# Performance work log

Measured on AMD Instinct MI355X. Metric: run time of the kernel, lower is better.

The kernel has to match this reference:

```python
import jax, jax.numpy as jnp
import numpy as np

BN_EPS = 1e-5


def setup_inputs() -> dict:
    key = jax.random.key(0)
    ks = jax.random.split(key, 9)
    N, C, T, V, S, INTER, OUT = 64, 64, 300, 25, 3, 16, 64
    return {
        "x": jax.random.normal(ks[0], (N, C, T, V), dtype=jnp.float32),
        "A": jax.random.uniform(ks[1], (S, V, V), dtype=jnp.float32),
        "PA": jax.random.normal(ks[2], (S, V, V), dtype=jnp.float32) * 1e-3,
        "Wa": jax.random.normal(ks[3], (S, INTER, C), dtype=jnp.float32) * 0.1,
        "ba": jax.random.normal(ks[4], (S, INTER), dtype=jnp.float32) * 0.1,
        "Wb": jax.random.normal(ks[5], (S, INTER, C), dtype=jnp.float32) * 0.1,
        "bb": jax.random.normal(ks[6], (S, INTER), dtype=jnp.float32) * 0.1,
        "Wd": jax.random.normal(ks[7], (S, OUT, C), dtype=jnp.float32) * 0.1,
        "bd": jax.random.normal(ks[8], (S, OUT), dtype=jnp.float32) * 0.1,
        "gamma": jnp.ones((OUT,), dtype=jnp.float32),
        "beta": jnp.zeros((OUT,), dtype=jnp.float32),
    }


def reference(x, A, PA, Wa, ba, Wb, bb, Wd, bd, gamma, beta):
    N, C, T, V = x.shape
    S, INTER = Wa.shape[0], Wa.shape[1]
    K = INTER * T  # contraction length for attention

    # 1x1 convs for all subsets at once: [N,S,inter,T,V]
    fa = jnp.einsum('nctv,sic->nsitv', x, Wa) + ba[None, :, :, None, None]
    fb = jnp.einsum('nctv,sic->nsitv', x, Wb) + bb[None, :, :, None, None]

    # A1: permute(0,3,1,2).view(N,V,inter*T)  -> [N,S,V,K]
    A1 = fa.transpose(0, 1, 4, 2, 3).reshape(N, S, V, K)
    # A2: view(N,inter*T,V)                   -> [N,S,K,V]
    A2 = fb.reshape(N, S, K, V)

    # attention: softmax over dim=-2, plus learned adjacency
    att = jnp.einsum('nsvk,nskw->nsvw', A1, A2) / jnp.asarray(K, x.dtype)
    att = jax.nn.softmax(att, axis=-2) + (A + PA)[None]  # [N,S,V,V]

    # message passing: x.view(N,C*T,V) @ att, then 1x1 conv_d, summed over subsets
    xm = jnp.einsum('nkv,nsvw->nskw', x.reshape(N, C * T, V), att)
    xm = xm.reshape(N, S, C, T, V)
    y = jnp.einsum('nsctv,soc->notv', xm, Wd) + bd.sum(0)[None, :, None, None]

    # BatchNorm2d (training-mode batch stats, per-channel over N,T,V)
    mean = y.mean(axis=(0, 2, 3), keepdims=True)
    var = y.var(axis=(0, 2, 3), keepdims=True)
    y = gamma[None, :, None, None] * (y - mean) * jax.lax.rsqrt(var + BN_EPS) \
        + beta[None, :, None, None]

    # residual (in_channels == out_channels -> identity down) + relu
    return jax.nn.relu(y + x)
```

## Files before the change

### kernel.cpp

```cpp
#include <hip/hip_runtime.h>
#include <math.h>

constexpr int Nn = 64, Cc = 64, Tt = 300, Vv = 25, Ss = 3, Ii = 16, Oo = 64;
constexpr int TVc  = Tt * Vv;
constexpr int CTVc = Cc * TVc;
constexpr float KINV = 1.0f / 4800.0f;

constexpr int WS_ATT  = 0;
constexpr int WS_SUM  = 120000;
constexpr int WS_SQ   = 120512;
constexpr int WS_MEAN = 121024;
constexpr int WS_RSTD = 121088;
constexpr int WS_ZERO_FLOATS = 121024;
constexpr int WS_XB_F   = 121152;
constexpr int WS_WAB_F  = WS_XB_F + 15360000;
constexpr int WS_WDB_F  = WS_WAB_F + 3072;
constexpr int WS_ATTB_F = WS_WDB_F + 6144;
constexpr int WS_END_F  = WS_ATTB_F + 98304;
constexpr size_t WS_NEED = (size_t)WS_END_F * 4;

typedef __attribute__((ext_vector_type(8))) short bf16x8;
typedef __attribute__((ext_vector_type(4))) short short4v;
typedef __attribute__((ext_vector_type(4))) float f32x4;
typedef __attribute__((ext_vector_type(16))) float f32x16;
typedef __attribute__((ext_vector_type(4))) int int4v;

__device__ __forceinline__ short f2bf(float f) {
    unsigned u = __builtin_bit_cast(unsigned, f);
    u += 0x7FFFu + ((u >> 16) & 1u);
    return (short)(u >> 16);
}
__device__ __forceinline__ float bf2f(short s) {
    unsigned u = ((unsigned)(unsigned short)s) << 16;
    return __builtin_bit_cast(float, u);
}
__device__ __forceinline__ void store4(float* p, f32x4 v) {
    __builtin_memcpy(p, &v, 16);
}

__global__ __launch_bounds__(256) void k0_xpose(
    const float* __restrict__ x, short* __restrict__ xb)
{
    const int n   = blockIdx.y;
    const int tid = threadIdx.x;
    const int tv  = blockIdx.x * 32 + (tid & 31);
    const int g   = (tid >> 5) & 7;
    if (tv >= TVc) return;
    const float* xp = x + (size_t)n * CTVc + (size_t)(g * 8) * TVc + tv;
    bf16x8 o;
    #pragma unroll
    for (int j = 0; j < 8; ++j) o[j] = f2bf(xp[(size_t)j * TVc]);
    *(bf16x8*)(xb + ((size_t)n * TVc + tv) * 64 + g * 8) = o;
}

__global__ __launch_bounds__(256) void kpack(
    const float* __restrict__ Wa, const float* __restrict__ Wb,
    const float* __restrict__ Wd, short* __restrict__ wab, short* __restrict__ wdb)
{
    const int i = blockIdx.x * 256 + threadIdx.x;
    if (i < 6144) {
        const int s = i >> 11, rb = i & 2047, r = rb >> 6, c = rb & 63;
        const float v = (r < 16) ? Wa[(s * 16 + r) * 64 + c]
                                 : Wb[(s * 16 + (r - 16)) * 64 + c];
        wab[i] = f2bf(v);
    }
    if (i < 12288) wdb[i] = f2bf(Wd[i]);
}

template<bool XB>
__device__ __forceinline__ void load_xfrag(
    const float* __restrict__ xn, const short* __restrict__ xbn,
    int tv, bool ok, int quad, bf16x8& b0, bf16x8& b1)
{
    if constexpr (XB) {
        const short* bp = xbn + (ok ? tv : 0) * 64 + quad * 8;
        b0 = *(const bf16x8*)bp;
        b1 = *(const bf16x8*)(bp + 32);
    } else {
        const float* bp = xn + (quad * 8) * TVc + tv;
        #pragma unroll
        for (int j = 0; j < 8; ++j) {
            b0[j] = f2bf(ok ? bp[j * TVc] : 0.0f);
            b1[j] = f2bf(ok ? bp[(j + 32) * TVc] : 0.0f);
        }
    }
}

template<bool XB>
__global__ __launch_bounds__(256) void ka_gram_mfma(
    const float* __restrict__ x, const short* __restrict__ xb,
    const short* __restrict__ wab,
    const float* __restrict__ Wa, const float* __restrict__ ba,
    const float* __restrict__ Wb, const float* __restrict__ bb,
    float* __restrict__ att)
{
    __shared__ short uT[112 * 104];
    __shared__ float part[4 * 1024];
    __shared__ float bab[96];

    const int tid = threadIdx.x;
    const int t0  = blockIdx.x * 4;
    const int n   = blockIdx.y;
    const float* xn  = x + n * CTVc + t0 * 25;
    const short* xbn = XB ? (xb + ((size_t)n * TVc + t0 * 25) * 64) : nullptr;

    if (tid < 96) {
        const int s = tid >> 5, r = tid & 31;
        bab[tid] = (r < 16) ? ba[s * 16 + r] : bb[s * 16 + r - 16];
    }

    const int lane = tid & 63;
    const int wave = tid >> 6;
    const int l16  = lane & 15;
    const int quad = lane >> 4;

    bf16x8 afr[3][2][2];
    #pragma unroll
    for (int s = 0; s < 3; ++s)
        #pragma unroll
        for (int half = 0; half < 2; ++half)
            #pragma unroll
            for (int k = 0; k < 2; ++k) {
                if constexpr (XB) {
                    afr[s][half][k] = *(const bf16x8*)(
                        wab + (s * 32 + half * 16 + l16) * 64 + k * 32 + quad * 8);
                } else {
                    const float* W = half ? Wb : Wa;
                    const float* wp = W + (s * 16 + l16) * 64 + k * 32 + quad * 8;
                    const float4 w0 = *(const float4*)wp;
                    const float4 w1 = *(const float4*)(wp + 4);
                    bf16x8 a;
                    a[0] = f2bf(w0.x); a[1] = f2bf(w0.y); a[2] = f2bf(w0.z); a[3] = f2bf(w0.w);
                    a[4] = f2bf(w1.x); a[5] = f2bf(w1.y); a[6] = f2bf(w1.z); a[7] = f2bf(w1.w);
                    afr[s][half][k] = a;
                }
            }
    __syncthreads();

    for (int nt = wave; nt < 7; nt += 4) {
        const int tv = nt * 16 + l16;
        const bool ok = tv < 100;
        bf16x8 b0, b1;
        load_xfrag<XB>(xn, xbn, tv, ok, quad, b0, b1);
        #pragma unroll
        for (int s = 0; s < 3; ++s)
            #pragma unroll
            for (int half = 0; half < 2; ++half) {
                f32x4 acc = {0.0f, 0.0f, 0.0f, 0.0f};
                acc = __builtin_amdgcn_mfma_f32_16x16x32_bf16(afr[s][half][0], b0, acc, 0, 0, 0);
                acc = __builtin_amdgcn_mfma_f32_16x16x32_bf16(afr[s][half][1], b1, acc, 0, 0, 0);
                const float4 bv = *(const float4*)(bab + s * 32 + half * 16 + quad * 4);
                short4v pk;
                pk[0] = f2bf(acc[0] + bv.x); pk[1] = f2bf(acc[1] + bv.y);
                pk[2] = f2bf(acc[2] + bv.z); pk[3] = f2bf(acc[3] + bv.w);
                *(short4v*)(uT + tv * 104 + s * 32 + half * 16 + quad * 4) = pk;
            }
    }
    __syncthreads();

    const int t   = wave;
    const int w32 = lane & 31;
    const int khi = lane >> 5;
    f32x16 g[3];
    #pragma unroll
    for (int s = 0; s < 3; ++s)
        #pragma unroll
        for (int r = 0; r < 16; ++r) g[s][r] = 0.0f;

    #pragma unroll
    for (int s = 0; s < 3; ++s) {
        const short* base = uT + (t * 25 + w32) * 104 + s * 32 + khi * 8;
        const bf16x8 aA = *(const bf16x8*)(base);
        const bf16x8 bB = *(const bf16x8*)(base + 16);
        g[s] = __builtin_amdgcn_mfma_f32_32x32x16_bf16(aA, bB, g[s], 0, 0, 0);
    }

    for (int s = 0; s < 3; ++s) {
        __syncthreads();
        #pragma unroll
        for (int r = 0; r < 16; ++r) {
            const int row = (r & 3) + 8 * (r >> 2) + 4 * khi;
            part[wave * 1024 + row * 32 + w32] = g[s][r];
        }
        __syncthreads();
        float* attns = att + (n * 3 + s) * 625;
        for (int p = tid; p < 625; p += 256) {
            const int v = p / 25, w = p - v * 25;
            const int q = v * 32 + w;
            atomicAdd(attns + p, part[q] + part[1024 + q] + part[2048 + q] + part[3072 + q]);
        }
    }
}

template<bool ATTB>
__global__ __launch_bounds__(64) void kb_softmax(
    float* __restrict__ att, const float* __restrict__ A, const float* __restrict__ PA,
    short* __restrict__ attb)
{
    const int b = blockIdx.x;
    const int s = b % 3;
    const int w = threadIdx.x;
    if (w >= 32) return;
    float col[25] = {};
    if (w < 25) {
        float* base = att + b * 625;
        float m = -1e30f;
        #pragma unroll
        for (int v = 0; v < 25; ++v) {
            col[v] = base[v * 25 + w] * KINV;
            m = fmaxf(m, col[v]);
        }
        float sum = 0.0f;
        #pragma unroll
        for (int v = 0; v < 25; ++v) { col[v] = expf(col[v] - m); sum += col[v]; }
        const float inv = 1.0f / sum;
        #pragma unroll
        for (int v = 0; v < 25; ++v) {
            col[v] = fmaf(col[v], inv, A[(s * 25 + v) * 25 + w] + PA[(s * 25 + v) * 25 + w]);
            base[v * 25 + w] = col[v];
        }
    }
    if constexpr (ATTB) {
        short* dst = attb + b * 1024 + w * 32;
        #pragma unroll
        for (int v = 0; v < 25; ++v) dst[v] = (w < 25) ? f2bf(col[v]) : (short)0;
        #pragma unroll
        for (int v = 25; v < 32; ++v) dst[v] = 0;
    }
}

constexpr int K3_TILES = 3;

__global__ __launch_bounds__(512, 6) void k3_y_mfma(
    const short* __restrict__ xb, const short* __restrict__ wdb,
    const short* __restrict__ attb, float* __restrict__ y, float* __restrict__ bns)
{
    __shared__ __align__(16) short U[192 * 128];
    __shared__ float bnA[8][32], bnB[8][32];

    const int tid = threadIdx.x;
    const int n   = blockIdx.y;
    const int tb0 = blockIdx.x * K3_TILES;

    const int lane = tid & 63;
    const int wave = tid >> 6;
    const int l16  = lane & 15;
    const int quad = lane >> 4;

    for (int i = tid; i < 3072; i += 512)
        ((int4v*)U)[i] = (int4v){0, 0, 0, 0};

    bf16x8 a0[3], a1[3];
    #pragma unroll
    for (int s = 0; s < 3; ++s) {
        const short* ab = attb + (size_t)(n * 3 + s) * 1024 + l16 * 32 + quad * 8;
        a0[s] = *(const bf16x8*)ab;
        a1[s] = *(const bf16x8*)(ab + 512);
    }

    const int tv  = (wave < 7) ? wave * 16 + l16 : 0;
    const bool ok = (wave < 7) && (tv < 100);
    const int tl  = tv / 25;
    const int vp  = tv - tl * 25;
    const int col = tl * 32 + vp;
    const int grp = col >> 3, ing = col & 7;

    const short* xtile = xb + ((size_t)n * TVc + tb0 * 100) * 64;
    const int xoff = (ok ? tv : 0) * 64 + quad * 8;

    bf16x8 bc0 = *(const bf16x8*)(xtile + xoff);
    bf16x8 bc1 = *(const bf16x8*)(xtile + xoff + 32);
    bf16x8 nx0, nx1;

    const int t  = wave >> 1;
    const int ob = (wave & 1) * 32;
    float s1[2] = {0.0f, 0.0f}, s2[2] = {0.0f, 0.0f};

    __syncthreads();

    #pragma unroll
    for (int it = 0; it < K3_TILES; ++it) {
        if (it + 1 < K3_TILES) {
            const short* bp = xtile + (it + 1) * 6400 + xoff;
            nx0 = *(const bf16x8*)bp;
            nx1 = *(const bf16x8*)(bp + 32);
        }

        if (wave < 7) {
            #pragma unroll
            for (int s = 0; s < 3; ++s)
                #pragma unroll
                for (int m = 0; m < 4; ++m) {
                    const short* wp = wdb + (s * 64 + m * 16 + l16) * 64 + quad * 8;
                    const bf16x8 f0 = *(const bf16x8*)wp;
                    const bf16x8 f1 = *(const bf16x8*)(wp + 32);
                    f32x4 acc = {0.0f, 0.0f, 0.0f, 0.0f};
                    acc = __builtin_amdgcn_mfma_f32_16x16x32_bf16(f0, bc0, acc, 0, 0, 0);
                    acc = __builtin_amdgcn_mfma_f32_16x16x32_bf16(f1, bc1, acc, 0, 0, 0);
                    if (ok) {
                        #pragma unroll
                        for (int r = 0; r < 4; ++r) {
                            const int row = s * 64 + m * 16 + quad * 4 + r;
                            U[row * 128 + (((grp ^ (row & 15)) << 3) | ing)] = f2bf(acc[r]);
                        }
                    }
                }
        }
        __syncthreads();

        f32x4 D[2][2];
        #pragma unroll
        for (int mt = 0; mt < 2; ++mt)
            #pragma unroll
            for (int nb = 0; nb < 2; ++nb) D[mt][nb] = (f32x4){0.0f, 0.0f, 0.0f, 0.0f};
        #pragma unroll
        for (int s = 0; s < 3; ++s) {
            #pragma unroll
            for (int nb = 0; nb < 2; ++nb) {
                const int row = s * 64 + ob + nb * 16 + l16;
                const bf16x8 bv = *(const bf16x8*)(
                    U + row * 128 + (((t * 4 + quad) ^ (row & 15)) << 3));
                D[0][nb] = __builtin_amdgcn_mfma_f32_16x16x32_bf16(a0[s], bv, D[0][nb], 0, 0, 0);
                D[1][nb] = __builtin_amdgcn_mfma_f32_16x16x32_bf16(a1[s], bv, D[1][nb], 0, 0, 0);
            }
        }

        const int t0 = (tb0 + it) * 4;
        #pragma unroll
        for (int nb = 0; nb < 2; ++nb) {
            const int og = ob + nb * 16 + l16;
            float* dst = y + ((size_t)(n * 64 + og) * 300 + t0 + t) * 25;
            const f32x4 d0 = D[0][nb];
            store4(dst + quad * 4, d0);
            s1[nb] += d0[0] + d0[1] + d0[2] + d0[3];
            s2[nb] += d0[0]*d0[0] + d0[1]*d0[1] + d0[2]*d0[2] + d0[3]*d0[3];
            const f32x4 d1 = D[1][nb];
            if (quad < 2) {
                store4(dst + 16 + quad * 4, d1);
                s1[nb] += d1[0] + d1[1] + d1[2] + d1[3];
                s2[nb] += d1[0]*d1[0] + d1[1]*d1[1] + d1[2]*d1[2] + d1[3]*d1[3];
            } else if (quad == 2) {
                dst[24] = d1[0];
                s1[nb] += d1[0];
                s2[nb] += d1[0] * d1[0];
            }
        }
        __syncthreads();
        if (it + 1 < K3_TILES) { bc0 = nx0; bc1 = nx1; }
    }

    #pragma unroll
    for (int nb = 0; nb < 2; ++nb) {
        s1[nb] += __shfl_xor(s1[nb], 16); s1[nb] += __shfl_xor(s1[nb], 32);
        s2[nb] += __shfl_xor(s2[nb], 16); s2[nb] += __shfl_xor(s2[nb], 32);
    }
    if (lane < 16) {
        bnA[wave][lane]      = s1[0];
        bnA[wave][16 + lane] = s1[1];
        bnB[wave][lane]      = s2[0];
        bnB[wave][16 + lane] = s2[1];
    }
    __syncthreads();
    if (tid < 64) {
        const int o = tid, h = o >> 5, i = o & 31;
        const float S1 = bnA[h][i] + bnA[h + 2][i] + bnA[h + 4][i] + bnA[h + 6][i];
        const float S2 = bnB[h][i] + bnB[h + 2][i] + bnB[h + 4][i] + bnB[h + 6][i];
        const int cp = (blockIdx.x & 7) * 64;
        atomicAdd(bns + cp + o, S1);
        atomicAdd(bns + 512 + cp + o, S2);
    }
}

__global__ __launch_bounds__(256) void k3_y_mfma_fb(
    const float* __restrict__ x, const float* __restrict__ Wd,
    const float* __restrict__ att, float* __restrict__ y, float* __restrict__ bns)
{
    __shared__ __align__(16) short U[96 * 128];
    __shared__ __align__(16) short attT[3 * 1024];
    __shared__ float bn1[4][32], bn2[4][32];

    const int tid = threadIdx.x;
    const int t0  = blockIdx.x * 4;
    const int n   = blockIdx.y;
    const int oh  = blockIdx.z;
    const float* xn = x + n * CTVc + t0 * 25;

    const int lane = tid & 63;
    const int wave = tid >> 6;
    const int l16  = lane & 15;
    const int quad = lane >> 4;

    for (int i = tid; i < 1536; i += 256)
        ((int4v*)U)[i] = (int4v){0, 0, 0, 0};
    for (int i = tid; i < 3072; i += 256) {
        const int s = i >> 10, r = i & 1023, v = r >> 5, vp = r & 31;
        const float val = (v < 25 && vp < 25) ? att[(n * 3 + s) * 625 + vp * 25 + v] : 0.0f;
        attT[i] = f2bf(val);
    }
    bf16x8 afr[3][2][2];
    #pragma unroll
    for (int s = 0; s < 3; ++s)
        #pragma unroll
        for (int m = 0; m < 2; ++m)
            #pragma unroll
            for (int k = 0; k < 2; ++k) {
                const float* wp = Wd + ((s * 64 + oh * 32 + m * 16 + l16) * 64) + k * 32 + quad * 8;
                const float4 w0 = *(const float4*)wp;
                const float4 w1 = *(const float4*)(wp + 4);
                bf16x8 a;
                a[0] = f2bf(w0.x); a[1] = f2bf(w0.y); a[2] = f2bf(w0.z); a[3] = f2bf(w0.w);
                a[4] = f2bf(w1.x); a[5] = f2bf(w1.y); a[6] = f2bf(w1.z); a[7] = f2bf(w1.w);
                afr[s][m][k] = a;
            }
    __syncthreads();

    for (int nt = wave; nt < 7; nt += 4) {
        const int tv = nt * 16 + l16;
        const bool ok = tv < 100;
        bf16x8 b0, b1;
        load_xfrag<false>(xn, nullptr, tv, ok, quad, b0, b1);
        const int tl  = tv / 25;
        const int vp  = tv - tl * 25;
        const int col = tl * 32 + vp;
        const int grp = col >> 3, ing = col & 7;
        #pragma unroll
        for (int s = 0; s < 3; ++s)
            #pragma unroll
            for (int m = 0; m < 2; ++m) {
                f32x4 acc = {0.0f, 0.0f, 0.0f, 0.0f};
                acc = __builtin_amdgcn_mfma_f32_16x16x32_bf16(afr[s][m][0], b0, acc, 0, 0, 0);
                acc = __builtin_amdgcn_mfma_f32_16x16x32_bf16(afr[s][m][1], b1, acc, 0, 0, 0);
                if (ok) {
                    #pragma unroll
                    for (int r = 0; r < 4; ++r) {
                        const int row = s * 32 + m * 16 + quad * 4 + r;
                        U[row * 128 + (((grp ^ (row & 15)) << 3) | ing)] = f2bf(acc[r]);
                    }
                }
            }
    }
    __syncthreads();

    const int t = wave;
    bf16x8 aF[3][2], bF[3][2];
    #pragma unroll
    for (int s = 0; s < 3; ++s) {
        #pragma unroll
        for (int mt = 0; mt < 2; ++mt)
            aF[s][mt] = *(const bf16x8*)(attT + s * 1024 + (mt * 16 + l16) * 32 + quad * 8);
        #pragma unroll
        for (int nb = 0; nb < 2; ++nb) {
            const int row = s * 32 + nb * 16 + l16;
            bF[s][nb] = *(const bf16x8*)(U + row * 128 + (((t * 4 + quad) ^ (row & 15)) << 3));
        }
    }
    f32x4 D[2][2];
    #pragma unroll
    for (int mt = 0; mt < 2; ++mt)
        #pragma unroll
        for (int nb = 0; nb < 2; ++nb) D[mt][nb] = (f32x4){0.0f, 0.0f, 0.0f, 0.0f};
    #pragma unroll
    for (int s = 0; s < 3; ++s)
        #pragma unroll
        for (int mt = 0; mt < 2; ++mt)
            #pragma unroll
            for (int nb = 0; nb < 2; ++nb)
                D[mt][nb] = __builtin_amdgcn_mfma_f32_16x16x32_bf16(aF[s][mt], bF[s][nb], D[mt][nb], 0, 0, 0);

    float s1[2] = {0.0f, 0.0f}, s2[2] = {0.0f, 0.0f};
    #pragma unroll
    for (int nb = 0; nb < 2; ++nb) {
        const int og = oh * 32 + nb * 16 + l16;
        float* dst = y + ((size_t)(n * 64 + og) * 300 + t0 + t) * 25;
        const f32x4 d0 = D[0][nb];
        store4(dst + quad * 4, d0);
        s1[nb] += d0[0] + d0[1] + d0[2] + d0[3];
        s2[nb] += d0[0]*d0[0] + d0[1]*d0[1] + d0[2]*d0[2] + d0[3]*d0[3];
        const f32x4 d1 = D[1][nb];
        if (quad < 2) {
            store4(dst + 16 + quad * 4, d1);
            s1[nb] += d1[0] + d1[1] + d1[2] + d1[3];
            s2[nb] += d1[0]*d1[0] + d1[1]*d1[1] + d1[2]*d1[2] + d1[3]*d1[3];
        } else if (quad == 2) {
            dst[24] = d1[0];
            s1[nb] += d1[0];
            s2[nb] += d1[0] * d1[0];
        }
    }
    #pragma unroll
    for (int nb = 0; nb < 2; ++nb) {
        s1[nb] += __shfl_xor(s1[nb], 16); s1[nb] += __shfl_xor(s1[nb], 32);
        s2[nb] += __shfl_xor(s2[nb], 16); s2[nb] += __shfl_xor(s2[nb], 32);
    }
    if (lane < 16) {
        bn1[wave][lane]      = s1[0];
        bn1[wave][16 + lane] = s1[1];
        bn2[wave][lane]      = s2[0];
        bn2[wave][16 + lane] = s2[1];
    }
    __syncthreads();
    if (tid < 32) {
        const float S1 = bn1[0][tid] + bn1[1][tid] + bn1[2][tid] + bn1[3][tid];
        const float S2 = bn2[0][tid] + bn2[1][tid] + bn2[2][tid] + bn2[3][tid];
        const int cp = (blockIdx.x & 7) * 64;
        atomicAdd(bns + cp + oh * 32 + tid, S1);
        atomicAdd(bns + 512 + cp + oh * 32 + tid, S2);
    }
}

__global__ __launch_bounds__(64) void k3b_stats(float* __restrict__ ws)
{
    const int o = threadIdx.x;
    if (o >= 64) return;
    const float cnt_inv = 1.0f / 480000.0f;
    float s = 0.0f, q = 0.0f;
    #pragma unroll
    for (int j = 0; j < 8; ++j) {
        s += ws[WS_SUM + j * 64 + o];
        q += ws[WS_SQ  + j * 64 + o];
    }
    const float mean = s * cnt_inv;
    const float var  = q * cnt_inv - mean * mean;
    ws[WS_MEAN + o] = mean;
    ws[WS_RSTD + o] = rsqrtf(var + 1e-5f);
}

__global__ __launch_bounds__(256) void k4_bn(
    float* __restrict__ out, const float* __restrict__ x,
    const float* __restrict__ gamma, const float* __restrict__ beta,
    const float* __restrict__ ws)
{
    const int o = blockIdx.y, n = blockIdx.z;
    const int j = blockIdx.x * 256 + threadIdx.x;
    if (j >= 1875) return;
    const size_t i4 = (size_t)(n * 64 + o) * 1875 + j;
    const float mean = ws[WS_MEAN + o], rstd = ws[WS_RSTD + o];
    const float g = gamma[o], b = beta[o];
    const float4 yv = ((const float4*)out)[i4];
    const float4 xv = ((const float4*)x)[i4];
    float4 r;
    r.x = fmaxf(fmaf(g * (yv.x - mean), rstd, b) + xv.x, 0.0f);
    r.y = fmaxf(fmaf(g * (yv.y - mean), rstd, b) + xv.y, 0.0f);
    r.z = fmaxf(fmaf(g * (yv.z - mean), rstd, b) + xv.z, 0.0f);
    r.w = fmaxf(fmaf(g * (yv.w - mean), rstd, b) + xv.w, 0.0f);
    ((float4*)out)[i4] = r;
}

extern "C" void kernel_launch(void* const* d_in, const int* in_sizes, int n_in,
                              void* d_out, int out_size, void* d_ws, size_t ws_size,
                              hipStream_t stream)
{
    const float* x  = (const float*)d_in[0];
    const float* A  = (const float*)d_in[1];
    const float* PA = (const float*)d_in[2];
    const float* Wa = (const float*)d_in[3];
    const float* ba = (const float*)d_in[4];
    const float* Wb = (const float*)d_in[5];
    const float* bb = (const float*)d_in[6];
    const float* Wd = (const float*)d_in[7];
    const float* gamma = (const float*)d_in[9];
    const float* beta  = (const float*)d_in[10];
    float* out = (float*)d_out;
    float* ws  = (float*)d_ws;

    hipMemsetAsync(d_ws, 0, (size_t)WS_ZERO_FLOATS * sizeof(float), stream);

    if (ws_size >= WS_NEED) {
        short* xbp  = (short*)(ws + WS_XB_F);
        short* wab  = (short*)(ws + WS_WAB_F);
        short* wdb  = (short*)(ws + WS_WDB_F);
        short* attb = (short*)(ws + WS_ATTB_F);
        k0_xpose<<<dim3(235, 64), 256, 0, stream>>>(x, xbp);
        kpack<<<dim3(48), 256, 0, stream>>>(Wa, Wb, Wd, wab, wdb);
        ka_gram_mfma<true><<<dim3(75, 64), 256, 0, stream>>>(
            x, xbp, wab, Wa, ba, Wb, bb, ws + WS_ATT);
        kb_softmax<true><<<dim3(192), 64, 0, stream>>>(ws + WS_ATT, A, PA, attb);
        k3_y_mfma<<<dim3(25, 64), 512, 0, stream>>>(xbp, wdb, attb, out, ws + WS_SUM);
    } else {
        ka_gram_mfma<false><<<dim3(75, 64), 256, 0, stream>>>(
            x, nullptr, nullptr, Wa, ba, Wb, bb, ws + WS_ATT);
        kb_softmax<false><<<dim3(192), 64, 0, stream>>>(ws + WS_ATT, A, PA, nullptr);
        k3_y_mfma_fb<<<dim3(75, 64, 2), 256, 0, stream>>>(
            x, Wd, ws + WS_ATT, out, ws + WS_SUM);
    }
    k3b_stats<<<dim3(1), 64, 0, stream>>>(ws);
    k4_bn<<<dim3(8, 64, 64), 256, 0, stream>>>(out, x, gamma, beta, ws);
}
```

Before: 499.6 us.

## Replace gram atomics with partial buffers, stage y through LDS, grid-stride BN

The attention gram kernel now writes per-tile partial 25x25 matrices to a workspace buffer instead of using atomicAdd. A new fused kernel reduces those partials, applies the softmax and writes the bf16 attention matrix. The y kernel handles one tile per block across 75x64 blocks, stages its output through LDS and writes it back with coalesced vector stores. The BN kernel becomes a grid-stride loop over a flat grid. These changes remove atomic contention and improve store coalescing, at the cost of an extra ~36MB partial buffer and the loss of the cross-tile prefetch in the y kernel.

```diff
diff --git a/kernel.cpp b/kernel.cpp
--- a/kernel.cpp
+++ b/kernel.cpp
@@ -18,6 +18,8 @@
 constexpr int WS_ATTB_F = WS_WDB_F + 6144;
 constexpr int WS_END_F  = WS_ATTB_F + 98304;
 constexpr size_t WS_NEED = (size_t)WS_END_F * 4;
+constexpr int WS_PART_F = WS_END_F;
+constexpr size_t WS_NEED2 = (size_t)(WS_PART_F + 9000000) * 4;
 
 typedef __attribute__((ext_vector_type(8))) short bf16x8;
 typedef __attribute__((ext_vector_type(4))) short short4v;
@@ -192,6 +194,99 @@
     }
 }
 
+__global__ __launch_bounds__(256) void ka_gram_part(
+    const short* __restrict__ xb, const short* __restrict__ wab,
+    const float* __restrict__ ba, const float* __restrict__ bb,
+    float* __restrict__ partp)
+{
+    __shared__ short uT[112 * 104];
+    __shared__ float part[4 * 1024];
+    __shared__ float bab[96];
+
+    const int tid = threadIdx.x;
+    const int bx  = blockIdx.x;
+    const int n   = blockIdx.y;
+    const short* xbn = xb + ((size_t)n * TVc + bx * 100) * 64;
+
+    if (tid < 96) {
+        const int s = tid >> 5, r = tid & 31;
+        bab[tid] = (r < 16) ? ba[s * 16 + r] : bb[s * 16 + r - 16];
+    }
+
+    const int lane = tid & 63;
+    const int wave = tid >> 6;
+    const int l16  = lane & 15;
+    const int quad = lane >> 4;
+
+    bf16x8 afr[3][2][2];
+    #pragma unroll
+    for (int s = 0; s < 3; ++s)
+        #pragma unroll
+        for (int half = 0; half < 2; ++half)
+            #pragma unroll
+            for (int k = 0; k < 2; ++k)
+                afr[s][half][k] = *(const bf16x8*)(
+                    wab + (s * 32 + half * 16 + l16) * 64 + k * 32 + quad * 8);
+    __syncthreads();
+
+    for (int nt = wave; nt < 7; nt += 4) {
+        const int tv = nt * 16 + l16;
+        const bool ok = tv < 100;
+        const short* bp = xbn + (ok ? tv : 0) * 64 + quad * 8;
+        const bf16x8 b0 = *(const bf16x8*)bp;
+        const bf16x8 b1 = *(const bf16x8*)(bp + 32);
+        #pragma unroll
+        for (int s = 0; s < 3; ++s)
+            #pragma unroll
+            for (int half = 0; half < 2; ++half) {
+                f32x4 acc = {0.0f, 0.0f, 0.0f, 0.0f};
+                acc = __builtin_amdgcn_mfma_f32_16x16x32_bf16(afr[s][half][0], b0, acc, 0, 0, 0);
+                acc = __builtin_amdgcn_mfma_f32_16x16x32_bf16(afr[s][half][1], b1, acc, 0, 0, 0);
+                const float4 bv = *(const float4*)(bab + s * 32 + half * 16 + quad * 4);
+                short4v pk;
+                pk[0] = f2bf(acc[0] + bv.x); pk[1] = f2bf(acc[1] + bv.y);
+                pk[2] = f2bf(acc[2] + bv.z); pk[3] = f2bf(acc[3] + bv.w);
+                if (ok)
+                    *(short4v*)(uT + tv * 104 + s * 32 + half * 16 + quad * 4) = pk;
+            }
+    }
+    __syncthreads();
+
+    const int t   = wave;
+    const int w32 = lane & 31;
+    const int khi = lane >> 5;
+    f32x16 g[3];
+    #pragma unroll
+    for (int s = 0; s < 3; ++s)
+        #pragma unroll
+        for (int r = 0; r < 16; ++r) g[s][r] = 0.0f;
+
+    #pragma unroll
+    for (int s = 0; s < 3; ++s) {
+        const short* base = uT + (t * 25 + w32) * 104 + s * 32 + khi * 8;
+        const bf16x8 aA = *(const bf16x8*)(base);
+        const bf16x8 bB = *(const bf16x8*)(base + 16);
+        g[s] = __builtin_amdgcn_mfma_f32_32x32x16_bf16(aA, bB, g[s], 0, 0, 0);
+    }
+
+    for (int s = 0; s < 3; ++s) {
+        __syncthreads();
+        #pragma unroll
+        for (int r = 0; r < 16; ++r) {
+            const int row = (r & 3) + 8 * (r >> 2) + 4 * khi;
+            part[wave * 1024 + row * 32 + w32] = g[s][r];
+        }
+        __syncthreads();
+        float* po = partp + ((size_t)(n * 75 + bx) * 3 + s) * 625;
+        for (int p = tid; p < 625; p += 256) {
+            const int v = p / 25, w = p - v * 25;
+            const int q = v * 32 + w;
+            po[p] = part[q] + part[1024 + q] + part[2048 + q] + part[3072 + q];
+        }
+    }
+}
+
+
 template<bool ATTB>
 __global__ __launch_bounds__(64) void kb_softmax(
     float* __restrict__ att, const float* __restrict__ A, const float* __restrict__ PA,
@@ -229,7 +324,49 @@
     }
 }
 
-constexpr int K3_TILES = 3;
+__global__ __launch_bounds__(256) void kb_fuse(
+    const float* __restrict__ partp, const float* __restrict__ A,
+    const float* __restrict__ PA, short* __restrict__ attb)
+{
+    __shared__ float att_s[625];
+    const int b = blockIdx.x;
+    const int n = b / 3, s = b - n * 3;
+    const int tid = threadIdx.x;
+
+    const float* pp = partp + (size_t)n * 75 * 1875 + s * 625;
+    for (int p = tid; p < 625; p += 256) {
+        float acc = 0.0f;
+        #pragma unroll 5
+        for (int bx = 0; bx < 75; ++bx) acc += pp[(size_t)bx * 1875 + p];
+        att_s[p] = acc;
+    }
+    __syncthreads();
+
+    if (tid < 32) {
+        const int w = tid;
+        float col[25] = {};
+        if (w < 25) {
+            float m = -1e30f;
+            #pragma unroll
+            for (int v = 0; v < 25; ++v) {
+                col[v] = att_s[v * 25 + w] * KINV;
+                m = fmaxf(m, col[v]);
+            }
+            float sum = 0.0f;
+            #pragma unroll
+            for (int v = 0; v < 25; ++v) { col[v] = expf(col[v] - m); sum += col[v]; }
+            const float inv = 1.0f / sum;
+            #pragma unroll
+            for (int v = 0; v < 25; ++v)
+                col[v] = fmaf(col[v], inv, A[(s * 25 + v) * 25 + w] + PA[(s * 25 + v) * 25 + w]);
+        }
+        short* dst = attb + b * 1024 + w * 32;
+        #pragma unroll
+        for (int v = 0; v < 25; ++v) dst[v] = (w < 25) ? f2bf(col[v]) : (short)0;
+        #pragma unroll
+        for (int v = 25; v < 32; ++v) dst[v] = 0;
+    }
+}
 
 __global__ __launch_bounds__(512, 6) void k3_y_mfma(
     const short* __restrict__ xb, const short* __restrict__ wdb,
@@ -239,16 +376,20 @@
     __shared__ float bnA[8][32], bnB[8][32];
 
     const int tid = threadIdx.x;
+    const int bx  = blockIdx.x;
     const int n   = blockIdx.y;
-    const int tb0 = blockIdx.x * K3_TILES;
 
     const int lane = tid & 63;
     const int wave = tid >> 6;
     const int l16  = lane & 15;
     const int quad = lane >> 4;
 
-    for (int i = tid; i < 3072; i += 512)
-        ((int4v*)U)[i] = (int4v){0, 0, 0, 0};
+    const int tv  = (wave < 7) ? wave * 16 + l16 : 0;
+    const bool ok = (wave < 7) && (tv < 100);
+    const short* xbn = xb + ((size_t)n * TVc + bx * 100) * 64;
+    const int xoff = (ok ? tv : 0) * 64 + quad * 8;
+    const bf16x8 bc0 = *(const bf16x8*)(xbn + xoff);
+    const bf16x8 bc1 = *(const bf16x8*)(xbn + xoff + 32);
 
     bf16x8 a0[3], a1[3];
     #pragma unroll
@@ -258,97 +399,80 @@
         a1[s] = *(const bf16x8*)(ab + 512);
     }
 
-    const int tv  = (wave < 7) ? wave * 16 + l16 : 0;
-    const bool ok = (wave < 7) && (tv < 100);
     const int tl  = tv / 25;
     const int vp  = tv - tl * 25;
     const int col = tl * 32 + vp;
     const int grp = col >> 3, ing = col & 7;
 
-    const short* xtile = xb + ((size_t)n * TVc + tb0 * 100) * 64;
-    const int xoff = (ok ? tv : 0) * 64 + quad * 8;
-
-    bf16x8 bc0 = *(const bf16x8*)(xtile + xoff);
-    bf16x8 bc1 = *(const bf16x8*)(xtile + xoff + 32);
-    bf16x8 nx0, nx1;
+    for (int i = tid; i < 3072; i += 512)
+        ((int4v*)U)[i] = (int4v){0, 0, 0, 0};
+    __syncthreads();
+
+    if (wave < 7) {
+        #pragma unroll
+        for (int s = 0; s < 3; ++s)
+            #pragma unroll
+            for (int m = 0; m < 4; ++m) {
+                const short* wp = wdb + (s * 64 + m * 16 + l16) * 64 + quad * 8;
+                const bf16x8 f0 = *(const bf16x8*)wp;
+                const bf16x8 f1 = *(const bf16x8*)(wp + 32);
+                f32x4 acc = {0.0f, 0.0f, 0.0f, 0.0f};
+                acc = __builtin_amdgcn_mfma_f32_16x16x32_bf16(f0, bc0, acc, 0, 0, 0);
+                acc = __builtin_amdgcn_mfma_f32_16x16x32_bf16(f1, bc1, acc, 0, 0, 0);
+                if (ok) {
+                    #pragma unroll
+                    for (int r = 0; r < 4; ++r) {
+                        const int row = s * 64 + m * 16 + quad * 4 + r;
+                        U[row * 128 + (((grp ^ (row & 15)) << 3) | ing)] = f2bf(acc[r]);
+                    }
+                }
+            }
+    }
+    __syncthreads();
 
     const int t  = wave >> 1;
     const int ob = (wave & 1) * 32;
+    f32x4 D[2][2];
+    #pragma unroll
+    for (int mt = 0; mt < 2; ++mt)
+        #pragma unroll
+        for (int nb = 0; nb < 2; ++nb) D[mt][nb] = (f32x4){0.0f, 0.0f, 0.0f, 0.0f};
+    #pragma unroll
+    for (int s = 0; s < 3; ++s) {
+        #pragma unroll
+        for (int nb = 0; nb < 2; ++nb) {
+            const int row = s * 64 + ob + nb * 16 + l16;
+            const bf16x8 bv = *(const bf16x8*)(
+                U + row * 128 + (((t * 4 + quad) ^ (row & 15)) << 3));
+            D[0][nb] = __builtin_amdgcn_mfma_f32_16x16x32_bf16(a0[s], bv, D[0][nb], 0, 0, 0);
+            D[1][nb] = __builtin_amdgcn_mfma_f32_16x16x32_bf16(a1[s], bv, D[1][nb], 0, 0, 0);
+        }
+    }
+    __syncthreads();
+
+    float* yS = (float*)U;
     float s1[2] = {0.0f, 0.0f}, s2[2] = {0.0f, 0.0f};
-
-    __syncthreads();
-
-    #pragma unroll
-    for (int it = 0; it < K3_TILES; ++it) {
-        if (it + 1 < K3_TILES) {
-            const short* bp = xtile + (it + 1) * 6400 + xoff;
-            nx0 = *(const bf16x8*)bp;
-            nx1 = *(const bf16x8*)(bp + 32);
-        }
-
-        if (wave < 7) {
-            #pragma unroll
-            for (int s = 0; s < 3; ++s)
-                #pragma unroll
-                for (int m = 0; m < 4; ++m) {
-                    const short* wp = wdb + (s * 64 + m * 16 + l16) * 64 + quad * 8;
-                    const bf16x8 f0 = *(const bf16x8*)wp;
-                    const bf16x8 f1 = *(const bf16x8*)(wp + 32);
-                    f32x4 acc = {0.0f, 0.0f, 0.0f, 0.0f};
-                    acc = __builtin_amdgcn_mfma_f32_16x16x32_bf16(f0, bc0, acc, 0, 0, 0);
-                    acc = __builtin_amdgcn_mfma_f32_16x16x32_bf16(f1, bc1, acc, 0, 0, 0);
-                    if (ok) {
-                        #pragma unroll
-                        for (int r = 0; r < 4; ++r) {
-                            const int row = s * 64 + m * 16 + quad * 4 + r;
-                            U[row * 128 + (((grp ^ (row & 15)) << 3) | ing)] = f2bf(acc[r]);
-                        }
-                    }
-                }
-        }
-        __syncthreads();
-
-        f32x4 D[2][2];
-        #pragma unroll
-        for (int mt = 0; mt < 2; ++mt)
-            #pragma unroll
-            for (int nb = 0; nb < 2; ++nb) D[mt][nb] = (f32x4){0.0f, 0.0f, 0.0f, 0.0f};
-        #pragma unroll
-        for (int s = 0; s < 3; ++s) {
-            #pragma unroll
-            for (int nb = 0; nb < 2; ++nb) {
-                const int row = s * 64 + ob + nb * 16 + l16;
-                const bf16x8 bv = *(const bf16x8*)(
-                    U + row * 128 + (((t * 4 + quad) ^ (row & 15)) << 3));
-                D[0][nb] = __builtin_amdgcn_mfma_f32_16x16x32_bf16(a0[s], bv, D[0][nb], 0, 0, 0);
-                D[1][nb] = __builtin_amdgcn_mfma_f32_16x16x32_bf16(a1[s], bv, D[1][nb], 0, 0, 0);
-            }
-        }
-
-        const int t0 = (tb0 + it) * 4;
-        #pragma unroll
-        for (int nb = 0; nb < 2; ++nb) {
-            const int og = ob + nb * 16 + l16;
-            float* dst = y + ((size_t)(n * 64 + og) * 300 + t0 + t) * 25;
-            const f32x4 d0 = D[0][nb];
-            store4(dst + quad * 4, d0);
-            s1[nb] += d0[0] + d0[1] + d0[2] + d0[3];
-            s2[nb] += d0[0]*d0[0] + d0[1]*d0[1] + d0[2]*d0[2] + d0[3]*d0[3];
-            const f32x4 d1 = D[1][nb];
-            if (quad < 2) {
-                store4(dst + 16 + quad * 4, d1);
-                s1[nb] += d1[0] + d1[1] + d1[2] + d1[3];
-                s2[nb] += d1[0]*d1[0] + d1[1]*d1[1] + d1[2]*d1[2] + d1[3]*d1[3];
-            } else if (quad == 2) {
-                dst[24] = d1[0];
-                s1[nb] += d1[0];
-                s2[nb] += d1[0] * d1[0];
-            }
-        }
-        __syncthreads();
-        if (it + 1 < K3_TILES) { bc0 = nx0; bc1 = nx1; }
-    }
-
+    #pragma unroll
+    for (int nb = 0; nb < 2; ++nb) {
+        const int og = ob + nb * 16 + l16;
+        const int base = og * 100 + t * 25;
+        const f32x4 d0 = D[0][nb];
+        #pragma unroll
+        for (int j = 0; j < 4; ++j) yS[base + quad * 4 + j] = d0[j];
+        s1[nb] += d0[0] + d0[1] + d0[2] + d0[3];
+        s2[nb] += d0[0]*d0[0] + d0[1]*d0[1] + d0[2]*d0[2] + d0[3]*d0[3];
+        const f32x4 d1 = D[1][nb];
+        if (quad < 2) {
+            #pragma unroll
+            for (int j = 0; j < 4; ++j) yS[base + 16 + quad * 4 + j] = d1[j];
+            s1[nb] += d1[0] + d1[1] + d1[2] + d1[3];
+            s2[nb] += d1[0]*d1[0] + d1[1]*d1[1] + d1[2]*d1[2] + d1[3]*d1[3];
+        } else if (quad == 2) {
+            yS[base + 24] = d1[0];
+            s1[nb] += d1[0];
+            s2[nb] += d1[0] * d1[0];
+        }
+    }
     #pragma unroll
     for (int nb = 0; nb < 2; ++nb) {
         s1[nb] += __shfl_xor(s1[nb], 16); s1[nb] += __shfl_xor(s1[nb], 32);
@@ -361,11 +485,22 @@
         bnB[wave][16 + lane] = s2[1];
     }
     __syncthreads();
+
+    {
+        f32x4* y4 = (f32x4*)y;
+        const f32x4* ysv = (const f32x4*)yS;
+        const size_t obase = (size_t)n * 64 * 1875 + (size_t)bx * 25;
+        for (int i4 = tid; i4 < 1600; i4 += 512) {
+            const int og = i4 / 25;
+            const int c4 = i4 - og * 25;
+            y4[obase + (size_t)og * 1875 + c4] = ysv[i4];
+        }
+    }
     if (tid < 64) {
         const int o = tid, h = o >> 5, i = o & 31;
         const float S1 = bnA[h][i] + bnA[h + 2][i] + bnA[h + 4][i] + bnA[h + 6][i];
         const float S2 = bnB[h][i] + bnB[h + 2][i] + bnB[h + 4][i] + bnB[h + 6][i];
-        const int cp = (blockIdx.x & 7) * 64;
+        const int cp = (bx & 7) * 64;
         atomicAdd(bns + cp + o, S1);
         atomicAdd(bns + 512 + cp + o, S2);
     }
@@ -530,20 +665,20 @@
     const float* __restrict__ gamma, const float* __restrict__ beta,
     const float* __restrict__ ws)
 {
-    const int o = blockIdx.y, n = blockIdx.z;
-    const int j = blockIdx.x * 256 + threadIdx.x;
-    if (j >= 1875) return;
-    const size_t i4 = (size_t)(n * 64 + o) * 1875 + j;
-    const float mean = ws[WS_MEAN + o], rstd = ws[WS_RSTD + o];
-    const float g = gamma[o], b = beta[o];
-    const float4 yv = ((const float4*)out)[i4];
-    const float4 xv = ((const float4*)x)[i4];
-    float4 r;
-    r.x = fmaxf(fmaf(g * (yv.x - mean), rstd, b) + xv.x, 0.0f);
-    r.y = fmaxf(fmaf(g * (yv.y - mean), rstd, b) + xv.y, 0.0f);
-    r.z = fmaxf(fmaf(g * (yv.z - mean), rstd, b) + xv.z, 0.0f);
-    r.w = fmaxf(fmaf(g * (yv.w - mean), rstd, b) + xv.w, 0.0f);
-    ((float4*)out)[i4] = r;
+    const int stride = gridDim.x * 256;
+    for (int i4 = blockIdx.x * 256 + threadIdx.x; i4 < 7680000; i4 += stride) {
+        const int o = (i4 / 1875) & 63;
+        const float mean = ws[WS_MEAN + o], rstd = ws[WS_RSTD + o];
+        const float g = gamma[o], b = beta[o];
+        const float4 yv = ((const float4*)out)[i4];
+        const float4 xv = ((const float4*)x)[i4];
+        float4 r;
+        r.x = fmaxf(fmaf(g * (yv.x - mean), rstd, b) + xv.x, 0.0f);
+        r.y = fmaxf(fmaf(g * (yv.y - mean), rstd, b) + xv.y, 0.0f);
+        r.z = fmaxf(fmaf(g * (yv.z - mean), rstd, b) + xv.z, 0.0f);
+        r.w = fmaxf(fmaf(g * (yv.w - mean), rstd, b) + xv.w, 0.0f);
+        ((float4*)out)[i4] = r;
+    }
 }
 
 extern "C" void kernel_launch(void* const* d_in, const int* in_sizes, int n_in,
@@ -563,9 +698,20 @@
     float* out = (float*)d_out;
     float* ws  = (float*)d_ws;
 
-    hipMemsetAsync(d_ws, 0, (size_t)WS_ZERO_FLOATS * sizeof(float), stream);
-
-    if (ws_size >= WS_NEED) {
+    if (ws_size >= WS_NEED2) {
+        hipMemsetAsync(ws + WS_SUM, 0, 1024 * sizeof(float), stream);
+        short* xbp  = (short*)(ws + WS_XB_F);
+        short* wab  = (short*)(ws + WS_WAB_F);
+        short* wdb  = (short*)(ws + WS_WDB_F);
+        short* attb = (short*)(ws + WS_ATTB_F);
+        float* partp = ws + WS_PART_F;
+        k0_xpose<<<dim3(235, 64), 256, 0, stream>>>(x, xbp);
+        kpack<<<dim3(48), 256, 0, stream>>>(Wa, Wb, Wd, wab, wdb);
+        ka_gram_part<<<dim3(75, 64), 256, 0, stream>>>(xbp, wab, ba, bb, partp);
+        kb_fuse<<<dim3(192), 256, 0, stream>>>(partp, A, PA, attb);
+        k3_y_mfma<<<dim3(75, 64), 512, 0, stream>>>(xbp, wdb, attb, out, ws + WS_SUM);
+    } else if (ws_size >= WS_NEED) {
+        hipMemsetAsync(d_ws, 0, (size_t)WS_ZERO_FLOATS * sizeof(float), stream);
         short* xbp  = (short*)(ws + WS_XB_F);
         short* wab  = (short*)(ws + WS_WAB_F);
         short* wdb  = (short*)(ws + WS_WDB_F);
@@ -575,8 +721,9 @@
         ka_gram_mfma<true><<<dim3(75, 64), 256, 0, stream>>>(
             x, xbp, wab, Wa, ba, Wb, bb, ws + WS_ATT);
         kb_softmax<true><<<dim3(192), 64, 0, stream>>>(ws + WS_ATT, A, PA, attb);
-        k3_y_mfma<<<dim3(25, 64), 512, 0, stream>>>(xbp, wdb, attb, out, ws + WS_SUM);
+        k3_y_mfma<<<dim3(75, 64), 512, 0, stream>>>(xbp, wdb, attb, out, ws + WS_SUM);
     } else {
+        hipMemsetAsync(d_ws, 0, (size_t)WS_ZERO_FLOATS * sizeof(float), stream);
         ka_gram_mfma<false><<<dim3(75, 64), 256, 0, stream>>>(
             x, nullptr, nullptr, Wa, ba, Wb, bb, ws + WS_ATT);
         kb_softmax<false><<<dim3(192), 64, 0, stream>>>(ws + WS_ATT, A, PA, nullptr);
@@ -584,5 +731,5 @@
             x, Wd, ws + WS_ATT, out, ws + WS_SUM);
     }
     k3b_stats<<<dim3(1), 64, 0, stream>>>(ws);
-    k4_bn<<<dim3(8, 64, 64), 256, 0, stream>>>(out, x, gamma, beta, ws);
-}
+    k4_bn<<<dim3(2048), 256, 0, stream>>>(out, x, gamma, beta, ws);
+}
```

Result: faster. 483.4 us (-3.2%).
